# Kernel optimization log

Measured on AMD Instinct MI355X. Metric: run time of the kernel, lower is better.

The kernel has to match this reference:

```python
import jax, jax.numpy as jnp
import numpy as np

D_MODEL = 1024
EXPAND = 2
D_INNER = D_MODEL * EXPAND
KERNEL = 4
EPS = 1e-5


def setup_inputs() -> dict:
    key = jax.random.key(0)
    ks = jax.random.split(key, 8)
    B, L = 2, 4096
    x = jax.random.normal(ks[0], (B, L, D_MODEL), dtype=jnp.float32)
    norm_w = jnp.ones((D_MODEL,), jnp.float32)
    norm_b = jnp.zeros((D_MODEL,), jnp.float32)
    # torch Linear weight layout [out, in]
    in_proj_w = jax.random.normal(ks[1], (2 * D_INNER, D_MODEL), jnp.float32) / np.sqrt(D_MODEL)
    # depthwise Conv1d weight [d_inner, 1, K]
    conv_w = jax.random.normal(ks[2], (D_INNER, 1, KERNEL), jnp.float32) / np.sqrt(KERNEL)
    conv_b = jax.random.normal(ks[3], (D_INNER,), jnp.float32) * 0.02
    gate_w = jax.random.normal(ks[4], (D_INNER, D_INNER), jnp.float32) / np.sqrt(D_INNER)
    gate_b = jnp.zeros((D_INNER,), jnp.float32)
    out_proj_w = jax.random.normal(ks[5], (D_MODEL, D_INNER), jnp.float32) / np.sqrt(D_INNER)
    return {"x": x, "norm_w": norm_w, "norm_b": norm_b, "in_proj_w": in_proj_w,
            "conv_w": conv_w, "conv_b": conv_b, "gate_w": gate_w, "gate_b": gate_b,
            "out_proj_w": out_proj_w}


def _layernorm(x, w, b):
    mu = jnp.mean(x, axis=-1, keepdims=True)
    var = jnp.var(x, axis=-1, keepdims=True)
    return (x - mu) * jax.lax.rsqrt(var + EPS) * w + b


def _glru(x, norm_w, norm_b, in_proj_w, conv_w, conv_b, gate_w, gate_b, out_proj_w):
    B, L, D = x.shape
    residual = x
    xn = _layernorm(x, norm_w, norm_b)
    xz = jnp.einsum('bld,ed->ble', xn, in_proj_w)  # [B,L,2*d_inner]
    x_inner, z = jnp.split(xz, 2, axis=-1)
    # causal depthwise conv: torch pads 3 both sides then slices [:L] == left-pad 3
    lhs = jnp.transpose(x_inner, (0, 2, 1))  # [B, C, L]
    conv = jax.lax.conv_general_dilated(
        lhs, conv_w, window_strides=(1,), padding=[(KERNEL - 1, 0)],
        feature_group_count=D_INNER,
        dimension_numbers=('NCH', 'OIH', 'NCH'))
    x_conv = jnp.transpose(conv, (0, 2, 1)) + conv_b  # [B, L, C]
    x_conv = jax.nn.silu(x_conv)
    a = jax.nn.sigmoid(jnp.einsum('blc,ec->ble', x_conv, gate_w) + gate_b)
    b = (1.0 - a) * x_conv
    # h_t = a_t * h_{t-1} + b_t, h_0 prior = 0 -> parallel associative scan
    def combine(e1, e2):
        a1, b1 = e1
        a2, b2 = e2
        return a1 * a2, a2 * b1 + b2
    _, y = jax.lax.associative_scan(combine, (a, b), axis=1)
    y = y * jax.nn.silu(z)
    return residual + jnp.einsum('blc,dc->bld', y, out_proj_w)


def reference(x, norm_w, norm_b, in_proj_w, conv_w, conv_b, gate_w, gate_b, out_proj_w):
    return _glru(x, norm_w, norm_b, in_proj_w, conv_w, conv_b, gate_w, gate_b, out_proj_w)
```

## Files before the change

### kernel.cpp

```cpp
#include <hip/hip_runtime.h>
#include <cstdint>

#define D_MODEL 1024
#define D_INNER 2048
#define LSEQ    4096
#define BATCH   2
#define M_ROWS  (BATCH * LSEQ)
#define CHUNK   128
#define NCHUNK  (LSEQ / CHUNK)

typedef unsigned short u16;
typedef __bf16 bf16x8 __attribute__((ext_vector_type(8)));
typedef float f32x4 __attribute__((ext_vector_type(4)));
typedef u16 u16x4 __attribute__((ext_vector_type(4)));

__device__ __forceinline__ u16 f2bf(float f) {
  union { float f; unsigned u; } x; x.f = f;
  unsigned u = x.u;
  unsigned r = (u + 0x7FFFu + ((u >> 16) & 1u)) >> 16;
  return (u16)r;
}
__device__ __forceinline__ float bf2f(u16 h) {
  union { unsigned u; float f; } x; x.u = ((unsigned)h) << 16;
  return x.f;
}
__device__ __forceinline__ float sigmoidf_(float v) { return 1.0f / (1.0f + expf(-v)); }
__device__ __forceinline__ float siluf_(float v)    { return v / (1.0f + expf(-v)); }

__device__ __forceinline__ void gl_lds16(const void* g, void* l) {
  __builtin_amdgcn_global_load_lds(
      (const __attribute__((address_space(1))) void*)g,
      (__attribute__((address_space(3))) void*)l, 16, 0, 0);
}

#define SBAR()   asm volatile("s_barrier" ::: "memory")
#define WAITV0() asm volatile("s_waitcnt vmcnt(0)" ::: "memory")
#define SGB()    __builtin_amdgcn_sched_barrier(0)

__global__ void __launch_bounds__(256)
cast3_kernel(const float* __restrict__ w0, const float* __restrict__ w1,
             const float* __restrict__ w2, u16* __restrict__ o0,
             u16* __restrict__ o1, u16* __restrict__ o2) {
  const int n04 = 2 * D_INNER * D_MODEL / 4;
  const int n14 = D_INNER * D_INNER / 4;
  const int n24 = D_MODEL * D_INNER / 4;
  int i = blockIdx.x * 256 + threadIdx.x;
  const float* src; u16* dst; int j;
  if (i < n04)            { src = w0; dst = o0; j = i; }
  else if (i < n04 + n14) { src = w1; dst = o1; j = i - n04; }
  else if (i < n04 + n14 + n24) { src = w2; dst = o2; j = i - n04 - n14; }
  else return;
  float4 v = ((const float4*)src)[j];
  u16x4 o;
  o.x = f2bf(v.x); o.y = f2bf(v.y); o.z = f2bf(v.z); o.w = f2bf(v.w);
  ((u16x4*)dst)[j] = o;
}

__global__ void __launch_bounds__(256)
ln_kernel(const float* __restrict__ x, const float* __restrict__ w,
          const float* __restrict__ b, u16* __restrict__ xn) {
  const int row = blockIdx.x;
  const int t = threadIdx.x;
  const float4 v = ((const float4*)(x + (size_t)row * D_MODEL))[t];
  float s  = v.x + v.y + v.z + v.w;
  float ss = v.x * v.x + v.y * v.y + v.z * v.z + v.w * v.w;
#pragma unroll
  for (int o = 32; o > 0; o >>= 1) {
    s  += __shfl_xor(s, o);
    ss += __shfl_xor(ss, o);
  }
  __shared__ float red[8];
  const int wid = t >> 6, lane = t & 63;
  if (lane == 0) { red[wid] = s; red[4 + wid] = ss; }
  __syncthreads();
  s  = red[0] + red[1] + red[2] + red[3];
  ss = red[4] + red[5] + red[6] + red[7];
  const float mu  = s * (1.0f / D_MODEL);
  const float var = ss * (1.0f / D_MODEL) - mu * mu;
  const float rs  = rsqrtf(var + 1e-5f);
  const float4 wv = ((const float4*)w)[t];
  const float4 bv = ((const float4*)b)[t];
  u16x4 o4;
  o4.x = f2bf((v.x - mu) * rs * wv.x + bv.x);
  o4.y = f2bf((v.y - mu) * rs * wv.y + bv.y);
  o4.z = f2bf((v.z - mu) * rs * wv.z + bv.z);
  o4.w = f2bf((v.w - mu) * rs * wv.w + bv.w);
  ((u16x4*)(xn + (size_t)row * D_MODEL))[t] = o4;
}

#define MFMA_BF16 __builtin_amdgcn_mfma_f32_16x16x32_bf16

template<int EPI, int BN>
__global__ void __launch_bounds__(512, 2)
gemmP(const u16* __restrict__ A, const u16* __restrict__ Bm,
      int M, int N, int K,
      const float* __restrict__ ef, float* __restrict__ of,
      u16* __restrict__ ob0, u16* __restrict__ ob1) {
  constexpr int NF  = BN / 64;
  constexpr int NF2 = NF / 2;
  constexpr int BBY = BN * 128;
  constexpr int BH  = BN / 128;
  __shared__ __align__(1024) char lds[65536 + 2 * BBY];
  const int tid = threadIdx.x, wid = tid >> 6, lane = tid & 63;
  const int nbx = N / BN;
  const int nwg = nbx * (M >> 8);
  const int bid = blockIdx.x;
  const int cpx = nwg >> 3;
  const int swzb = (bid & 7) * cpx + (bid >> 3);
  const int bx = swzb % nbx, by = swzb / nbx;
  const size_t m0 = (size_t)by << 8;
  const size_t n0 = (size_t)bx * BN;
  const int wr = wid >> 2, wc = wid & 3;
  const size_t rb = (size_t)K * 2;

  const int strow = lane >> 3;
  const int stchk = (lane & 7) ^ strow;
  const char* gA = (const char*)A  + (m0 + (size_t)(wid * 8 + strow)) * rb + stchk * 16;
  const char* gB = (const char*)Bm + (n0 + (size_t)(wid * 8 + strow)) * rb + stchk * 16;
  const int sdw = wid * 1024;

  auto ST_A = [&](int t) {
    char* d = lds + (t & 1) * 32768 + sdw;
    const char* s = gA + (size_t)t * 128;
#pragma unroll
    for (int h = 0; h < 2; ++h) {
      gl_lds16(s + (size_t)(h * 128) * rb,      d + h * 16384);
      gl_lds16(s + (size_t)(h * 128 + 64) * rb, d + h * 16384 + 8192);
    }
  };
  auto ST_B = [&](int t) {
    char* d = lds + 65536 + (t & 1) * BBY + sdw;
    const char* s = gB + (size_t)t * 128;
#pragma unroll
    for (int h = 0; h < BH; ++h) {
      gl_lds16(s + (size_t)(h * 128) * rb,      d + h * 16384);
      gl_lds16(s + (size_t)(h * 128 + 64) * rb, d + h * 16384 + 8192);
    }
  };

  const int q = lane >> 4, r15 = lane & 15;
  const int kx0 = ((q ^ (r15 & 7)) << 4);
  const int kx1 = (((4 + q) ^ (r15 & 7)) << 4);
  const int arow = r15 * 128;
  const int bwoff = (BN == 256) ? ((wc >> 1) * 16384) : 0;
  const int brow  = (BN == 256) ? (((wc & 1) * 64 + r15) * 128)
                                : ((wc * 32 + r15) * 128);

  bf16x8 af0[8], af1[8], b01[NF2], b23[NF2], c01[NF2], c23[NF2];
  f32x4 acc[8][NF] = {};

#define RDA(dst, kx, base) _Pragma("unroll") \
  for (int mf = 0; mf < 8; ++mf) dst[mf] = *(const bf16x8*)((base) + mf * 2048 + arow + (kx));
#define RDB(dst, kx, base, nf0) _Pragma("unroll") \
  for (int nf = 0; nf < NF2; ++nf) dst[nf] = *(const bf16x8*)((base) + (nf0 + nf) * 2048 + brow + (kx));
#define MM(afr, bfr, nf0) do { __builtin_amdgcn_s_setprio(1); _Pragma("unroll") \
  for (int mf = 0; mf < 8; ++mf) _Pragma("unroll") \
    for (int nf = 0; nf < NF2; ++nf) \
      acc[mf][nf0 + nf] = MFMA_BF16(afr[mf], bfr[nf], acc[mf][nf0 + nf], 0, 0, 0); \
  __builtin_amdgcn_s_setprio(0); } while (0)

  const int nk = K >> 6;

  ST_A(0); ST_B(0);
  WAITV0();
  SBAR();
  {
    const char* Ab = lds + wr * 16384;
    const char* Bb = lds + 65536 + bwoff;
    RDA(af0, kx0, Ab);
    RDB(b01, kx0, Bb, 0);
  }

  for (int t = 0; t < nk; ++t) {
    const int p = t & 1;
    const char* Ab = lds + p * 32768 + wr * 16384;
    const char* Bb = lds + 65536 + p * BBY + bwoff;
    const char* An = lds + (p ^ 1) * 32768 + wr * 16384;
    const char* Bn = lds + 65536 + (p ^ 1) * BBY + bwoff;
    const bool pf = (t + 1 < nk);

    if (pf) ST_A(t + 1);
    RDB(b23, kx0, Bb, NF2);
    SGB();
    MM(af0, b01, 0);
    SGB();

    if (pf) ST_B(t + 1);
    RDA(af1, kx1, Ab);
    RDB(c01, kx1, Bb, 0);
    SGB();
    MM(af0, b23, NF2);
    SGB();

    RDB(c23, kx1, Bb, NF2);
    SGB();
    MM(af1, c01, 0);
    SGB();

    MM(af1, c23, NF2);
    if (pf) {
      WAITV0();
      SBAR();
      RDA(af0, kx0, An);
      RDB(b01, kx0, Bn, 0);
    }
  }

#undef RDA
#undef RDB
#undef MM

  const int c0 = lane & 15;
  const int r0 = (lane >> 4) << 2;
  const bool isz = (EPI == 0) && (n0 >= (size_t)D_INNER);
#pragma unroll
  for (int mf = 0; mf < 8; ++mf) {
#pragma unroll
    for (int nf = 0; nf < NF; ++nf) {
#pragma unroll
      for (int rg = 0; rg < 4; ++rg) {
        const size_t row = m0 + (size_t)(wr * 128 + mf * 16 + r0 + rg);
        const size_t col = n0 + (size_t)(wc * (BN / 4) + nf * 16 + c0);
        const float v = acc[mf][nf][rg];
        if (EPI == 0) {
          if (!isz) ob0[row * D_INNER + col] = f2bf(v);
          else      ob1[row * D_INNER + (col - D_INNER)] = f2bf(siluf_(v));
        } else if (EPI == 1) {
          ob0[row * (size_t)N + col] = f2bf(v);
        } else {
          of[row * (size_t)N + col] = v + ef[row * (size_t)N + col];
        }
      }
    }
  }
}

__global__ void __launch_bounds__(256)
conv_silu_kernel(const u16* __restrict__ xin, const float* __restrict__ cw,
                 const float* __restrict__ cb, u16* __restrict__ xc) {
  const int c   = blockIdx.x * 256 + threadIdx.x;
  const int l0  = blockIdx.y * 8;
  const int bat = blockIdx.z;
  const size_t base = ((size_t)bat * LSEQ) * D_INNER + c;
  const float w0 = cw[c * 4 + 0], w1 = cw[c * 4 + 1], w2 = cw[c * 4 + 2], w3 = cw[c * 4 + 3];
  const float bb = cb[c];
  float v[11];
#pragma unroll
  for (int i = 0; i < 11; ++i) {
    const int l = l0 - 3 + i;
    v[i] = (l >= 0) ? bf2f(xin[base + (size_t)l * D_INNER]) : 0.0f;
  }
#pragma unroll
  for (int r = 0; r < 8; ++r) {
    const float acc = bb + w0 * v[r] + w1 * v[r + 1] + w2 * v[r + 2] + w3 * v[r + 3];
    xc[base + (size_t)(l0 + r) * D_INNER] = f2bf(siluf_(acc));
  }
}

__global__ void __launch_bounds__(256)
scan_a_kernel(const u16* __restrict__ g, const u16* __restrict__ xc,
              const float* __restrict__ gbias,
              float* __restrict__ cA, float* __restrict__ cB) {
  const int c   = (blockIdx.x * 256 + threadIdx.x) * 2;
  const int ch  = blockIdx.y;
  const int bat = blockIdx.z;
  const float bb0 = gbias[c], bb1 = gbias[c + 1];
  size_t idx = ((size_t)bat * LSEQ + (size_t)ch * CHUNK) * D_INNER + c;
  float pA0 = 1.0f, hB0 = 0.0f, pA1 = 1.0f, hB1 = 0.0f;
  for (int t = 0; t < CHUNK; ++t) {
    const ushort2 gg = *(const ushort2*)(g + idx);
    const ushort2 xx = *(const ushort2*)(xc + idx);
    const float a0 = sigmoidf_(bf2f(gg.x) + bb0);
    const float a1 = sigmoidf_(bf2f(gg.y) + bb1);
    pA0 *= a0; hB0 = a0 * hB0 + (1.0f - a0) * bf2f(xx.x);
    pA1 *= a1; hB1 = a1 * hB1 + (1.0f - a1) * bf2f(xx.y);
    idx += D_INNER;
  }
  const size_t o = ((size_t)bat * NCHUNK + ch) * D_INNER + c;
  *(float2*)(cA + o) = make_float2(pA0, pA1);
  *(float2*)(cB + o) = make_float2(hB0, hB1);
}

__global__ void __launch_bounds__(256)
scan_b_kernel(const float* __restrict__ cA, const float* __restrict__ cB,
              float* __restrict__ carry) {
  const int tid = blockIdx.x * 256 + threadIdx.x;
  const int bat = tid >> 11;
  const int c   = tid & (D_INNER - 1);
  float h = 0.0f;
  const size_t base = (size_t)bat * NCHUNK * D_INNER + c;
  for (int i = 0; i < NCHUNK; ++i) {
    const size_t o = base + (size_t)i * D_INNER;
    carry[o] = h;
    h = cA[o] * h + cB[o];
  }
}

__global__ void __launch_bounds__(256)
scan_c_kernel(const u16* __restrict__ g, const u16* __restrict__ xc,
              const u16* __restrict__ sz, const float* __restrict__ gbias,
              const float* __restrict__ carry, u16* __restrict__ yg) {
  const int c   = (blockIdx.x * 256 + threadIdx.x) * 2;
  const int ch  = blockIdx.y;
  const int bat = blockIdx.z;
  const float bb0 = gbias[c], bb1 = gbias[c + 1];
  const float2 h2 = *(const float2*)(carry + ((size_t)bat * NCHUNK + ch) * D_INNER + c);
  float h0 = h2.x, h1 = h2.y;
  size_t idx = ((size_t)bat * LSEQ + (size_t)ch * CHUNK) * D_INNER + c;
  for (int t = 0; t < CHUNK; ++t) {
    const ushort2 gg = *(const ushort2*)(g + idx);
    const ushort2 xx = *(const ushort2*)(xc + idx);
    const ushort2 zz = *(const ushort2*)(sz + idx);
    const float a0 = sigmoidf_(bf2f(gg.x) + bb0);
    const float a1 = sigmoidf_(bf2f(gg.y) + bb1);
    h0 = a0 * h0 + (1.0f - a0) * bf2f(xx.x);
    h1 = a1 * h1 + (1.0f - a1) * bf2f(xx.y);
    ushort2 o2;
    o2.x = f2bf(h0 * bf2f(zz.x));
    o2.y = f2bf(h1 * bf2f(zz.y));
    *(ushort2*)(yg + idx) = o2;
    idx += D_INNER;
  }
}

extern "C" void kernel_launch(void* const* d_in, const int* in_sizes, int n_in,
                              void* d_out, int out_size, void* d_ws, size_t ws_size,
                              hipStream_t stream) {
  const float* x         = (const float*)d_in[0];
  const float* norm_w    = (const float*)d_in[1];
  const float* norm_b    = (const float*)d_in[2];
  const float* in_proj_w = (const float*)d_in[3];
  const float* conv_w    = (const float*)d_in[4];
  const float* conv_b    = (const float*)d_in[5];
  const float* gate_w    = (const float*)d_in[6];
  const float* gate_b    = (const float*)d_in[7];
  const float* out_proj_w= (const float*)d_in[8];
  float* out = (float*)d_out;

  char* p = (char*)d_ws;
  u16* xn      = (u16*)p; p += (size_t)M_ROWS * D_MODEL * 2;
  u16* w_in    = (u16*)p; p += (size_t)2 * D_INNER * D_MODEL * 2;
  u16* w_gate  = (u16*)p; p += (size_t)D_INNER * D_INNER * 2;
  u16* w_out   = (u16*)p; p += (size_t)D_MODEL * D_INNER * 2;
  u16* x_inner = (u16*)p; p += (size_t)M_ROWS * D_INNER * 2;
  u16* szb     = (u16*)p; p += (size_t)M_ROWS * D_INNER * 2;
  u16* xconv   = (u16*)p; p += (size_t)M_ROWS * D_INNER * 2;
  u16* gbuf    = (u16*)p; p += (size_t)M_ROWS * D_INNER * 2;
  u16* yg      = (u16*)p; p += (size_t)M_ROWS * D_INNER * 2;
  float* cA    = (float*)p; p += (size_t)BATCH * NCHUNK * D_INNER * 4;
  float* cB    = (float*)p; p += (size_t)BATCH * NCHUNK * D_INNER * 4;
  float* carry = (float*)p; p += (size_t)BATCH * NCHUNK * D_INNER * 4;
  if ((size_t)(p - (char*)d_ws) > ws_size) return;

  const int ncast4 = (2 * D_INNER * D_MODEL + D_INNER * D_INNER + D_MODEL * D_INNER) / 4;
  cast3_kernel<<<dim3((ncast4 + 255) / 256), 256, 0, stream>>>(
      in_proj_w, gate_w, out_proj_w, w_in, w_gate, w_out);

  ln_kernel<<<dim3(M_ROWS), 256, 0, stream>>>(x, norm_w, norm_b, xn);

  gemmP<0, 256><<<dim3((M_ROWS / 256) * (2 * D_INNER / 256)), 512, 0, stream>>>(
      xn, w_in, M_ROWS, 2 * D_INNER, D_MODEL, nullptr, nullptr, x_inner, szb);

  conv_silu_kernel<<<dim3(D_INNER / 256, LSEQ / 8, BATCH), 256, 0, stream>>>(x_inner, conv_w, conv_b, xconv);

  gemmP<1, 256><<<dim3((M_ROWS / 256) * (D_INNER / 256)), 512, 0, stream>>>(
      xconv, w_gate, M_ROWS, D_INNER, D_INNER, nullptr, nullptr, gbuf, nullptr);

  scan_a_kernel<<<dim3(D_INNER / 512, NCHUNK, BATCH), 256, 0, stream>>>(gbuf, xconv, gate_b, cA, cB);
  scan_b_kernel<<<dim3(BATCH * D_INNER / 256), 256, 0, stream>>>(cA, cB, carry);
  scan_c_kernel<<<dim3(D_INNER / 512, NCHUNK, BATCH), 256, 0, stream>>>(gbuf, xconv, szb, gate_b, carry, yg);

  gemmP<2, 128><<<dim3((M_ROWS / 256) * (D_MODEL / 128)), 512, 0, stream>>>(
      yg, w_out, M_ROWS, D_MODEL, D_INNER, x, out, nullptr, nullptr);
}
```

Before: 323.3 us.

## Split-K out_proj GEMM with 256-wide tiles and halve scan chunk size

The out_proj GEMM now uses 256-wide N tiles and splits K into two halves over blockIdx.y. Each half writes bf16 partials, and a new reduce kernel sums them and adds the residual. The aim is more workgroups for the small-N GEMM (the same 256 as before, with larger tiles) and one shared GEMM template. The scan chunk also drops from 128 to 64, so the scan kernels have more parallelism. In exchange this adds an extra kernel, extra partial traffic, and a bf16 rounding of the partials before accumulation.

Measured after the change: 303.2 us. -6.2%, faster.

```diff
diff --git a/kernel.cpp b/kernel.cpp
--- a/kernel.cpp
+++ b/kernel.cpp
@@ -6,7 +6,7 @@
 #define LSEQ    4096
 #define BATCH   2
 #define M_ROWS  (BATCH * LSEQ)
-#define CHUNK   128
+#define CHUNK   64
 #define NCHUNK  (LSEQ / CHUNK)
 
 typedef unsigned short u16;
@@ -90,16 +90,13 @@
 
 #define MFMA_BF16 __builtin_amdgcn_mfma_f32_16x16x32_bf16
 
-template<int EPI, int BN>
+template<int EPI>
 __global__ void __launch_bounds__(512, 2)
 gemmP(const u16* __restrict__ A, const u16* __restrict__ Bm,
-      int M, int N, int K,
+      int M, int N, int K, int Kfull,
       const float* __restrict__ ef, float* __restrict__ of,
       u16* __restrict__ ob0, u16* __restrict__ ob1) {
-  constexpr int NF  = BN / 64;
-  constexpr int NF2 = NF / 2;
-  constexpr int BBY = BN * 128;
-  constexpr int BH  = BN / 128;
+  constexpr int BN = 256, NF = 4, NF2 = 2, BBY = BN * 128, BH = BN / 128;
   __shared__ __align__(1024) char lds[65536 + 2 * BBY];
   const int tid = threadIdx.x, wid = tid >> 6, lane = tid & 63;
   const int nbx = N / BN;
@@ -111,12 +108,13 @@
   const size_t m0 = (size_t)by << 8;
   const size_t n0 = (size_t)bx * BN;
   const int wr = wid >> 2, wc = wid & 3;
-  const size_t rb = (size_t)K * 2;
+  const size_t rb = (size_t)Kfull * 2;
+  const size_t kofs = (size_t)blockIdx.y * (size_t)K * 2;
 
   const int strow = lane >> 3;
   const int stchk = (lane & 7) ^ strow;
-  const char* gA = (const char*)A  + (m0 + (size_t)(wid * 8 + strow)) * rb + stchk * 16;
-  const char* gB = (const char*)Bm + (n0 + (size_t)(wid * 8 + strow)) * rb + stchk * 16;
+  const char* gA = (const char*)A  + (m0 + (size_t)(wid * 8 + strow)) * rb + stchk * 16 + kofs;
+  const char* gB = (const char*)Bm + (n0 + (size_t)(wid * 8 + strow)) * rb + stchk * 16 + kofs;
   const int sdw = wid * 1024;
 
   auto ST_A = [&](int t) {
@@ -142,9 +140,8 @@
   const int kx0 = ((q ^ (r15 & 7)) << 4);
   const int kx1 = (((4 + q) ^ (r15 & 7)) << 4);
   const int arow = r15 * 128;
-  const int bwoff = (BN == 256) ? ((wc >> 1) * 16384) : 0;
-  const int brow  = (BN == 256) ? (((wc & 1) * 64 + r15) * 128)
-                                : ((wc * 32 + r15) * 128);
+  const int bwoff = (wc >> 1) * 16384;
+  const int brow  = ((wc & 1) * 64 + r15) * 128;
 
   bf16x8 af0[8], af1[8], b01[NF2], b23[NF2], c01[NF2], c23[NF2];
   f32x4 acc[8][NF] = {};
@@ -213,6 +210,7 @@
   const int c0 = lane & 15;
   const int r0 = (lane >> 4) << 2;
   const bool isz = (EPI == 0) && (n0 >= (size_t)D_INNER);
+  u16* ob0p = (EPI == 1) ? (ob0 + (size_t)blockIdx.y * (size_t)M * N) : ob0;
 #pragma unroll
   for (int mf = 0; mf < 8; ++mf) {
 #pragma unroll
@@ -220,19 +218,35 @@
 #pragma unroll
       for (int rg = 0; rg < 4; ++rg) {
         const size_t row = m0 + (size_t)(wr * 128 + mf * 16 + r0 + rg);
-        const size_t col = n0 + (size_t)(wc * (BN / 4) + nf * 16 + c0);
+        const size_t col = n0 + (size_t)(wc * 64 + nf * 16 + c0);
         const float v = acc[mf][nf][rg];
         if (EPI == 0) {
           if (!isz) ob0[row * D_INNER + col] = f2bf(v);
           else      ob1[row * D_INNER + (col - D_INNER)] = f2bf(siluf_(v));
         } else if (EPI == 1) {
-          ob0[row * (size_t)N + col] = f2bf(v);
+          ob0p[row * (size_t)N + col] = f2bf(v);
         } else {
           of[row * (size_t)N + col] = v + ef[row * (size_t)N + col];
         }
       }
     }
   }
+}
+
+__global__ void __launch_bounds__(256)
+reduce3_kernel(const u16* __restrict__ part, const float* __restrict__ x,
+               float* __restrict__ out) {
+  const size_t MN = (size_t)M_ROWS * D_MODEL;
+  const size_t i = ((size_t)blockIdx.x * 256 + threadIdx.x) * 4;
+  const u16x4 a = *(const u16x4*)(part + i);
+  const u16x4 b = *(const u16x4*)(part + MN + i);
+  const float4 xv = *(const float4*)(x + i);
+  float4 o;
+  o.x = bf2f(a.x) + bf2f(b.x) + xv.x;
+  o.y = bf2f(a.y) + bf2f(b.y) + xv.y;
+  o.z = bf2f(a.z) + bf2f(b.z) + xv.z;
+  o.w = bf2f(a.w) + bf2f(b.w) + xv.w;
+  *(float4*)(out + i) = o;
 }
 
 __global__ void __launch_bounds__(256)
@@ -347,6 +361,7 @@
   u16* xconv   = (u16*)p; p += (size_t)M_ROWS * D_INNER * 2;
   u16* gbuf    = (u16*)p; p += (size_t)M_ROWS * D_INNER * 2;
   u16* yg      = (u16*)p; p += (size_t)M_ROWS * D_INNER * 2;
+  u16* part    = (u16*)p; p += (size_t)2 * M_ROWS * D_MODEL * 2;
   float* cA    = (float*)p; p += (size_t)BATCH * NCHUNK * D_INNER * 4;
   float* cB    = (float*)p; p += (size_t)BATCH * NCHUNK * D_INNER * 4;
   float* carry = (float*)p; p += (size_t)BATCH * NCHUNK * D_INNER * 4;
@@ -358,18 +373,21 @@
 
   ln_kernel<<<dim3(M_ROWS), 256, 0, stream>>>(x, norm_w, norm_b, xn);
 
-  gemmP<0, 256><<<dim3((M_ROWS / 256) * (2 * D_INNER / 256)), 512, 0, stream>>>(
-      xn, w_in, M_ROWS, 2 * D_INNER, D_MODEL, nullptr, nullptr, x_inner, szb);
-
-  conv_silu_kernel<<<dim3(D_INNER / 256, LSEQ / 8, BATCH), 256, 0, stream>>>(x_inner, conv_w, conv_b, xconv);
-
-  gemmP<1, 256><<<dim3((M_ROWS / 256) * (D_INNER / 256)), 512, 0, stream>>>(
-      xconv, w_gate, M_ROWS, D_INNER, D_INNER, nullptr, nullptr, gbuf, nullptr);
+  gemmP<0><<<dim3((M_ROWS / 256) * (2 * D_INNER / 256)), 512, 0, stream>>>(
+      xn, w_in, M_ROWS, 2 * D_INNER, D_MODEL, D_MODEL, nullptr, nullptr, x_inner, szb);
+
+  conv_silu_kernel<<<dim3(D_INNER / 256, LSEQ / 8, BATCH), 256, 0, stream>>>(
+      x_inner, conv_w, conv_b, xconv);
+
+  gemmP<1><<<dim3((M_ROWS / 256) * (D_INNER / 256)), 512, 0, stream>>>(
+      xconv, w_gate, M_ROWS, D_INNER, D_INNER, D_INNER, nullptr, nullptr, gbuf, nullptr);
 
   scan_a_kernel<<<dim3(D_INNER / 512, NCHUNK, BATCH), 256, 0, stream>>>(gbuf, xconv, gate_b, cA, cB);
   scan_b_kernel<<<dim3(BATCH * D_INNER / 256), 256, 0, stream>>>(cA, cB, carry);
   scan_c_kernel<<<dim3(D_INNER / 512, NCHUNK, BATCH), 256, 0, stream>>>(gbuf, xconv, szb, gate_b, carry, yg);
 
-  gemmP<2, 128><<<dim3((M_ROWS / 256) * (D_MODEL / 128)), 512, 0, stream>>>(
-      yg, w_out, M_ROWS, D_MODEL, D_INNER, x, out, nullptr, nullptr);
-}
+  gemmP<1><<<dim3((M_ROWS / 256) * (D_MODEL / 256), 2), 512, 0, stream>>>(
+      yg, w_out, M_ROWS, D_MODEL, D_INNER / 2, D_INNER, nullptr, nullptr, part, nullptr);
+
+  reduce3_kernel<<<dim3(M_ROWS * D_MODEL / 4 / 256), 256, 0, stream>>>(part, x, out);
+}
```
